# Kernel tuning notes

Hardware: AMD Instinct MI355X
Metric: run time of the kernel (lower is better)

Reference implementation:

```python
import jax, jax.numpy as jnp
import numpy as np

B, T, D, H = 512, 1024, 64, 64     # batch, time, input_size, hidden_size
R = 4                              # number of reward heads
MH = 32                            # MLP hidden size


def setup_inputs() -> dict:
    key = jax.random.key(0)
    ks = jax.random.split(key, 16)
    s = lambda k, shape, scale=1.0: jax.random.normal(k, shape, dtype=jnp.float32) * scale
    inp = {
        "x": s(ks[0], (B, T, D)),
        # learned initial states (nn.Parameter randn(1,1,H) -> store as (H,))
        "h_init": s(ks[1], (H,)),
        "c_init": s(ks[2], (H,)),
        # LSTM params, PyTorch layout: W_ih (4H, D), W_hh (4H, H), gate order i,f,g,o
        "W_ih": s(ks[3], (4 * H, D), 1.0 / np.sqrt(H)),
        "W_hh": s(ks[4], (4 * H, H), 1.0 / np.sqrt(H)),
        "b_ih": s(ks[5], (4 * H,), 1.0 / np.sqrt(H)),
        "b_hh": s(ks[6], (4 * H,), 1.0 / np.sqrt(H)),
        # R stacked MLP heads: Linear(H,MH) -> ReLU -> Linear(MH,MH) -> ReLU -> Linear(MH,1)
        "W1": s(ks[7], (R, MH, H), 1.0 / np.sqrt(H)),
        "b1": s(ks[8], (R, MH), 1.0 / np.sqrt(H)),
        "W2": s(ks[9], (R, MH, MH), 1.0 / np.sqrt(MH)),
        "b2": s(ks[10], (R, MH), 1.0 / np.sqrt(MH)),
        "W3": s(ks[11], (R, 1, MH), 1.0 / np.sqrt(MH)),
        "b3": s(ks[12], (R, 1), 1.0 / np.sqrt(MH)),
    }
    return inp


def _lstm(x, h0, c0, W_ih, W_hh, b_ih, b_hh):
    # x: (B, T, D). Returns y: (B, T, H).
    Hh = h0.shape[-1]
    b = b_ih + b_hh                      # (4H,)
    # precompute input projections for all steps: (T, B, 4H)
    xg = jnp.einsum('btd,gd->tbg', x, W_ih) + b

    def step(carry, xg_t):
        h, c = carry                     # (B, H) each
        gates = xg_t + h @ W_hh.T        # (B, 4H)
        i, f, g, o = jnp.split(gates, 4, axis=-1)
        c = jax.nn.sigmoid(f) * c + jax.nn.sigmoid(i) * jnp.tanh(g)
        h = jax.nn.sigmoid(o) * jnp.tanh(c)
        return (h, c), h

    Bb = x.shape[0]
    h0b = jnp.broadcast_to(h0, (Bb, Hh))
    c0b = jnp.broadcast_to(c0, (Bb, Hh))
    _, ys = jax.lax.scan(step, (h0b, c0b), xg)   # ys: (T, B, H)
    return jnp.transpose(ys, (1, 0, 2))


def _heads(y, W1, b1, W2, b2, W3, b3):
    # y: (B, T, H) -> (R, B, T); all R heads computed in one batched einsum chain
    h1 = jax.nn.relu(jnp.einsum('bth,rmh->rbtm', y, W1) + b1[:, None, None, :])
    h2 = jax.nn.relu(jnp.einsum('rbtm,rnm->rbtn', h1, W2) + b2[:, None, None, :])
    out = jnp.einsum('rbtn,ron->rbto', h2, W3) + b3[:, None, None, :]
    return out[..., 0]                   # squeeze last dim -> (R, B, T)


def reference(x, h_init, c_init, W_ih, W_hh, b_ih, b_hh, W1, b1, W2, b2, W3, b3):
    y = _lstm(x, h_init, c_init, W_ih, W_hh, b_ih, b_hh)
    outs = _heads(y, W1, b1, W2, b2, W3, b3)   # (R, B, T); row r == rewards[r] head
    return (y, outs)
```

## Files before the change

### kernel.cpp

```cpp
#include <hip/hip_runtime.h>

#define BB 512
#define TT 1024
#define DD 64
#define HH 64
#define G4 256
#define RR 4
#define MHH 32
#define BT (BB * TT)
#define Y_SIZE (BB * TT * HH)

typedef _Float16 half8 __attribute__((ext_vector_type(8)));
typedef _Float16 half4 __attribute__((ext_vector_type(4)));
typedef float f32x4 __attribute__((ext_vector_type(4)));

#define MFMA16(a, b, c) __builtin_amdgcn_mfma_f32_16x16x32_f16((a), (b), (c), 0, 0, 0)

__device__ __forceinline__ void wg_barrier_lds() {
    asm volatile("s_waitcnt lgkmcnt(0)" ::: "memory");
    __builtin_amdgcn_s_barrier();
    asm volatile("" ::: "memory");
}

__device__ __forceinline__ float sigm(float x) {
    return __builtin_amdgcn_rcpf(1.0f + __expf(-x));
}
__device__ __forceinline__ float tanh_(float x) {
    return 1.0f - 2.0f * __builtin_amdgcn_rcpf(1.0f + __expf(2.0f * x));
}

__device__ __forceinline__ half8 cvt8(f32x4 a, f32x4 b) {
    half8 h;
    h[0] = (_Float16)a[0]; h[1] = (_Float16)a[1];
    h[2] = (_Float16)a[2]; h[3] = (_Float16)a[3];
    h[4] = (_Float16)b[0]; h[5] = (_Float16)b[1];
    h[6] = (_Float16)b[2]; h[7] = (_Float16)b[3];
    return h;
}

__global__ __launch_bounds__(256) void lstm_kernel(
    const float* __restrict__ x, const float* __restrict__ h_init,
    const float* __restrict__ c_init, const float* __restrict__ W_ih,
    const float* __restrict__ W_hh, const float* __restrict__ b_ih,
    const float* __restrict__ b_hh, float* __restrict__ y)
{
    __shared__ alignas(16) _Float16 xch[2][16][2][DD];
    __shared__ alignas(16) _Float16 hst[2][2][HH];

    const int tid  = threadIdx.x;
    const int wave = tid >> 6;
    const int lane = tid & 63;
    const int col  = lane & 15;
    const int quad = lane >> 4;
    const int sel  = (lane >> 3) & 1;
    const int r_act = lane >> 5;
    const int j    = (wave << 4) + col;
    const bool writer = ((lane >> 4) & 1) == 0;

    const int b0 = blockIdx.x * 2;

    half8 bf[4][4];
    f32x4 biasv[4];
#pragma unroll
    for (int G = 0; G < 4; ++G) {
        const int n = (G << 6) + j;
        const float bs = b_ih[n] + b_hh[n];
        biasv[G][0] = bs; biasv[G][1] = bs; biasv[G][2] = bs; biasv[G][3] = bs;
#pragma unroll
        for (int c = 0; c < 4; ++c) {
            const float* src = (c < 2) ? (W_ih + n * DD + c * 32 + quad * 8)
                                       : (W_hh + n * HH + (c - 2) * 32 + quad * 8);
            f32x4 w0 = *(const f32x4*)src;
            f32x4 w1 = *(const f32x4*)(src + 4);
            bf[G][c] = cvt8(w0, w1);
        }
    }

    float c_state = c_init[j];

    if (tid < 128) {
        const int rr = tid >> 6, jj = tid & 63;
        hst[0][rr][jj] = (_Float16)h_init[jj];
    }
    {
        const int ss = tid >> 4, rr = (tid >> 3) & 1, j0 = (tid & 7) << 3;
        const float* src = x + ((b0 + rr) * TT + ss) * DD + j0;
        f32x4 g0 = *(const f32x4*)src;
        f32x4 g1 = *(const f32x4*)(src + 4);
        *(half8*)&xch[0][ss][rr][j0] = cvt8(g0, g1);
    }
    wg_barrier_lds();

    const int ss_pf = tid >> 4, rr_pf = (tid >> 3) & 1, j0_pf = (tid & 7) << 3;

    for (int ci = 0; ci < 64; ++ci) {
        const int buf = ci & 1;
        const bool pf = (ci + 1) < 64;
        f32x4 g0, g1;
        if (pf) {
            const float* src = x + ((b0 + rr_pf) * TT + ((ci + 1) << 4) + ss_pf) * DD + j0_pf;
            g0 = *(const f32x4*)src;
            g1 = *(const f32x4*)(src + 4);
        }
#pragma unroll
        for (int s = 0; s < 16; ++s) {
            const int t = (ci << 4) + s;
            const int p = s & 1;
            const _Float16* xrow = &xch[buf][s][sel][0];
            half8 a0 = *(const half8*)(xrow + quad * 8);
            half8 a1 = *(const half8*)(xrow + 32 + quad * 8);
            const _Float16* hrow = &hst[p][sel][0];
            half8 a2 = *(const half8*)(hrow + quad * 8);
            half8 a3 = *(const half8*)(hrow + 32 + quad * 8);

            f32x4 acc0 = MFMA16(a0, bf[0][0], biasv[0]);
            f32x4 acc1 = MFMA16(a0, bf[1][0], biasv[1]);
            f32x4 acc2 = MFMA16(a0, bf[2][0], biasv[2]);
            f32x4 acc3 = MFMA16(a0, bf[3][0], biasv[3]);
            acc0 = MFMA16(a1, bf[0][1], acc0); acc1 = MFMA16(a1, bf[1][1], acc1);
            acc2 = MFMA16(a1, bf[2][1], acc2); acc3 = MFMA16(a1, bf[3][1], acc3);
            acc0 = MFMA16(a2, bf[0][2], acc0); acc1 = MFMA16(a2, bf[1][2], acc1);
            acc2 = MFMA16(a2, bf[2][2], acc2); acc3 = MFMA16(a2, bf[3][2], acc3);
            acc0 = MFMA16(a3, bf[0][3], acc0); acc1 = MFMA16(a3, bf[1][3], acc1);
            acc2 = MFMA16(a3, bf[2][3], acc2); acc3 = MFMA16(a3, bf[3][3], acc3);

            const float si = sigm(acc0[0]);
            const float sf = sigm(acc1[0]);
            const float tg = tanh_(acc2[0]);
            const float so = sigm(acc3[0]);
            c_state = sf * c_state + si * tg;
            const float hv = so * tanh_(c_state);
            if (writer) {
                hst[p ^ 1][r_act][j] = (_Float16)hv;
                y[((b0 + r_act) * TT + t) * HH + j] = hv;
            }
            if (s == 15 && pf) {
                *(half8*)&xch[buf ^ 1][ss_pf][rr_pf][j0_pf] = cvt8(g0, g1);
            }
            wg_barrier_lds();
        }
    }
}

__global__ __launch_bounds__(256) void heads_kernel(
    const float* __restrict__ y,
    const float* __restrict__ W1, const float* __restrict__ b1,
    const float* __restrict__ W2, const float* __restrict__ b2,
    const float* __restrict__ W3, const float* __restrict__ b3,
    float* __restrict__ outs)
{
    __shared__ alignas(16) _Float16 ybuf[64][72];
    __shared__ alignas(16) _Float16 h1buf[64][136];
    __shared__ alignas(16) _Float16 h2buf[64][136];

    const int tid  = threadIdx.x;
    const int wave = tid >> 6;
    const int lane = tid & 63;
    const int col  = lane & 15;
    const int quad = lane >> 4;
    const int arow = (wave << 4) + col;

    half8 w1f[8][2]; float bias1[8];
#pragma unroll
    for (int nt = 0; nt < 8; ++nt) {
        const int n = nt * 16 + col;
        bias1[nt] = b1[n];
#pragma unroll
        for (int c = 0; c < 2; ++c) {
            const float* src = W1 + n * 64 + c * 32 + quad * 8;
            w1f[nt][c] = cvt8(*(const f32x4*)src, *(const f32x4*)(src + 4));
        }
    }
    half8 w2f[8]; float bias2[8];
#pragma unroll
    for (int nt = 0; nt < 8; ++nt) {
        const int n = nt * 16 + col;
        bias2[nt] = b2[n];
        const float* src = W2 + n * 32 + quad * 8;
        w2f[nt] = cvt8(*(const f32x4*)src, *(const f32x4*)(src + 4));
    }
    const int hd3 = tid >> 6, row3 = tid & 63;
    float w3r[32];
#pragma unroll
    for (int i = 0; i < 32; i += 4) {
        f32x4 v = *(const f32x4*)(W3 + hd3 * 32 + i);
        w3r[i] = v[0]; w3r[i + 1] = v[1]; w3r[i + 2] = v[2]; w3r[i + 3] = v[3];
    }
    const float b3v = b3[hd3];

    for (int st = 0; st < 4; ++st) {
        const long base_row = (long)blockIdx.x * 256 + st * 64;
#pragma unroll
        for (int jj = 0; jj < 4; ++jj) {
            const int off = (jj * 256 + tid) * 4;
            const int row = off >> 6, cc = off & 63;
            f32x4 v = *(const f32x4*)(y + base_row * 64 + off);
            half4 hv = {(_Float16)v[0], (_Float16)v[1], (_Float16)v[2], (_Float16)v[3]};
            *(half4*)&ybuf[row][cc] = hv;
        }
        wg_barrier_lds();

        half8 a0 = *(const half8*)&ybuf[arow][quad * 8];
        half8 a1 = *(const half8*)&ybuf[arow][32 + quad * 8];
#pragma unroll
        for (int nt = 0; nt < 8; ++nt) {
            f32x4 acc = {bias1[nt], bias1[nt], bias1[nt], bias1[nt]};
            acc = MFMA16(a0, w1f[nt][0], acc);
            acc = MFMA16(a1, w1f[nt][1], acc);
#pragma unroll
            for (int r = 0; r < 4; ++r) {
                float v = acc[r] > 0.0f ? acc[r] : 0.0f;
                h1buf[(wave << 4) + (quad << 2) + r][nt * 16 + col] = (_Float16)v;
            }
        }
        wg_barrier_lds();

        half8 ah[4];
#pragma unroll
        for (int hd = 0; hd < 4; ++hd)
            ah[hd] = *(const half8*)&h1buf[arow][hd * 32 + quad * 8];
#pragma unroll
        for (int nt = 0; nt < 8; ++nt) {
            f32x4 acc = {bias2[nt], bias2[nt], bias2[nt], bias2[nt]};
            acc = MFMA16(ah[nt >> 1], w2f[nt], acc);
#pragma unroll
            for (int r = 0; r < 4; ++r) {
                float v = acc[r] > 0.0f ? acc[r] : 0.0f;
                h2buf[(wave << 4) + (quad << 2) + r][nt * 16 + col] = (_Float16)v;
            }
        }
        wg_barrier_lds();

        float acc = b3v;
#pragma unroll
        for (int c = 0; c < 4; ++c) {
            half8 v = *(const half8*)&h2buf[row3][hd3 * 32 + c * 8];
#pragma unroll
            for (int u = 0; u < 8; ++u)
                acc = fmaf((float)v[u], w3r[c * 8 + u], acc);
        }
        outs[(long)hd3 * BT + base_row + row3] = acc;
        wg_barrier_lds();
    }
}

extern "C" void kernel_launch(void* const* d_in, const int* in_sizes, int n_in,
                              void* d_out, int out_size, void* d_ws, size_t ws_size,
                              hipStream_t stream) {
    (void)in_sizes; (void)n_in; (void)out_size; (void)d_ws; (void)ws_size;
    const float* x      = (const float*)d_in[0];
    const float* h_init = (const float*)d_in[1];
    const float* c_init = (const float*)d_in[2];
    const float* W_ih   = (const float*)d_in[3];
    const float* W_hh   = (const float*)d_in[4];
    const float* b_ih   = (const float*)d_in[5];
    const float* b_hh   = (const float*)d_in[6];
    const float* W1     = (const float*)d_in[7];
    const float* b1     = (const float*)d_in[8];
    const float* W2     = (const float*)d_in[9];
    const float* b2     = (const float*)d_in[10];
    const float* W3     = (const float*)d_in[11];
    const float* b3     = (const float*)d_in[12];
    float* y    = (float*)d_out;
    float* outs = y + Y_SIZE;

    lstm_kernel<<<dim3(256), dim3(256), 0, stream>>>(x, h_init, c_init, W_ih, W_hh,
                                                     b_ih, b_hh, y);
    heads_kernel<<<dim3(2048), dim3(256), 0, stream>>>(y, W1, b1, W2, b2, W3, b3, outs);
}
```

Baseline: 563.9 us.

## Hoist LSTM input projection per chunk and restructure heads kernel per-wave

The LSTM kernel now computes the input-projection MFMAs for a 16-step chunk up front into an LDS fp32 buffer, so each recurrent step only runs the four W_hh MFMAs on the critical path plus LDS reads of the precomputed gates. The x-chunk LDS rows are padded, and the prefetch store moves to step 14. The heads kernel is restructured so each wave processes its own rows with per-wave double-buffered LDS and no workgroup barriers. It loads y directly into registers with a one-tile prefetch, and the final W3 layer runs as an MFMA with zero-padded weights instead of scalar FMAs. This adds LDS usage and extra LDS traffic for the gate buffer.

```diff
diff --git a/kernel.cpp b/kernel.cpp
--- a/kernel.cpp
+++ b/kernel.cpp
@@ -4,9 +4,6 @@
 #define TT 1024
 #define DD 64
 #define HH 64
-#define G4 256
-#define RR 4
-#define MHH 32
 #define BT (BB * TT)
 #define Y_SIZE (BB * TT * HH)
 
@@ -44,8 +41,9 @@
     const float* __restrict__ W_hh, const float* __restrict__ b_ih,
     const float* __restrict__ b_hh, float* __restrict__ y)
 {
-    __shared__ alignas(16) _Float16 xch[2][16][2][DD];
+    __shared__ alignas(16) _Float16 xch[2][16][2][72];
     __shared__ alignas(16) _Float16 hst[2][2][HH];
+    __shared__ float xg[16][2][265];
 
     const int tid  = threadIdx.x;
     const int wave = tid >> 6;
@@ -102,25 +100,42 @@
             g0 = *(const f32x4*)src;
             g1 = *(const f32x4*)(src + 4);
         }
+
+#pragma unroll
+        for (int rr = 0; rr < 2; ++rr) {
+            half8 ax0 = *(const half8*)&xch[buf][col][rr][quad * 8];
+            half8 ax1 = *(const half8*)&xch[buf][col][rr][32 + quad * 8];
+#pragma unroll
+            for (int G = 0; G < 4; ++G) {
+                f32x4 d = MFMA16(ax0, bf[G][0], biasv[G]);
+                d = MFMA16(ax1, bf[G][1], d);
+#pragma unroll
+                for (int r = 0; r < 4; ++r)
+                    xg[(quad << 2) + r][rr][(G << 6) + j] = d[r];
+            }
+        }
+
 #pragma unroll
         for (int s = 0; s < 16; ++s) {
             const int t = (ci << 4) + s;
             const int p = s & 1;
-            const _Float16* xrow = &xch[buf][s][sel][0];
-            half8 a0 = *(const half8*)(xrow + quad * 8);
-            half8 a1 = *(const half8*)(xrow + 32 + quad * 8);
+
+            const float xg0 = xg[s][r_act][0 * 64 + j];
+            const float xg1 = xg[s][r_act][1 * 64 + j];
+            const float xg2 = xg[s][r_act][2 * 64 + j];
+            const float xg3 = xg[s][r_act][3 * 64 + j];
             const _Float16* hrow = &hst[p][sel][0];
             half8 a2 = *(const half8*)(hrow + quad * 8);
             half8 a3 = *(const half8*)(hrow + 32 + quad * 8);
 
-            f32x4 acc0 = MFMA16(a0, bf[0][0], biasv[0]);
-            f32x4 acc1 = MFMA16(a0, bf[1][0], biasv[1]);
-            f32x4 acc2 = MFMA16(a0, bf[2][0], biasv[2]);
-            f32x4 acc3 = MFMA16(a0, bf[3][0], biasv[3]);
-            acc0 = MFMA16(a1, bf[0][1], acc0); acc1 = MFMA16(a1, bf[1][1], acc1);
-            acc2 = MFMA16(a1, bf[2][1], acc2); acc3 = MFMA16(a1, bf[3][1], acc3);
-            acc0 = MFMA16(a2, bf[0][2], acc0); acc1 = MFMA16(a2, bf[1][2], acc1);
-            acc2 = MFMA16(a2, bf[2][2], acc2); acc3 = MFMA16(a2, bf[3][2], acc3);
+            f32x4 c0 = {xg0, xg0, xg0, xg0};
+            f32x4 c1 = {xg1, xg1, xg1, xg1};
+            f32x4 c2 = {xg2, xg2, xg2, xg2};
+            f32x4 c3 = {xg3, xg3, xg3, xg3};
+            f32x4 acc0 = MFMA16(a2, bf[0][2], c0);
+            f32x4 acc1 = MFMA16(a2, bf[1][2], c1);
+            f32x4 acc2 = MFMA16(a2, bf[2][2], c2);
+            f32x4 acc3 = MFMA16(a2, bf[3][2], c3);
             acc0 = MFMA16(a3, bf[0][3], acc0); acc1 = MFMA16(a3, bf[1][3], acc1);
             acc2 = MFMA16(a3, bf[2][3], acc2); acc3 = MFMA16(a3, bf[3][3], acc3);
 
@@ -134,7 +149,7 @@
                 hst[p ^ 1][r_act][j] = (_Float16)hv;
                 y[((b0 + r_act) * TT + t) * HH + j] = hv;
             }
-            if (s == 15 && pf) {
+            if (s == 14 && pf) {
                 *(half8*)&xch[buf ^ 1][ss_pf][rr_pf][j0_pf] = cvt8(g0, g1);
             }
             wg_barrier_lds();
@@ -149,16 +164,14 @@
     const float* __restrict__ W3, const float* __restrict__ b3,
     float* __restrict__ outs)
 {
-    __shared__ alignas(16) _Float16 ybuf[64][72];
-    __shared__ alignas(16) _Float16 h1buf[64][136];
-    __shared__ alignas(16) _Float16 h2buf[64][136];
+    __shared__ alignas(16) _Float16 h1w[4][2][16][144];
+    __shared__ alignas(16) _Float16 h2w[4][2][16][144];
 
     const int tid  = threadIdx.x;
     const int wave = tid >> 6;
     const int lane = tid & 63;
     const int col  = lane & 15;
     const int quad = lane >> 4;
-    const int arow = (wave << 4) + col;
 
     half8 w1f[8][2]; float bias1[8];
 #pragma unroll
@@ -179,29 +192,39 @@
         const float* src = W2 + n * 32 + quad * 8;
         w2f[nt] = cvt8(*(const f32x4*)src, *(const f32x4*)(src + 4));
     }
-    const int hd3 = tid >> 6, row3 = tid & 63;
-    float w3r[32];
-#pragma unroll
-    for (int i = 0; i < 32; i += 4) {
-        f32x4 v = *(const f32x4*)(W3 + hd3 * 32 + i);
-        w3r[i] = v[0]; w3r[i + 1] = v[1]; w3r[i + 2] = v[2]; w3r[i + 3] = v[3];
-    }
-    const float b3v = b3[hd3];
-
-    for (int st = 0; st < 4; ++st) {
-        const long base_row = (long)blockIdx.x * 256 + st * 64;
-#pragma unroll
-        for (int jj = 0; jj < 4; ++jj) {
-            const int off = (jj * 256 + tid) * 4;
-            const int row = off >> 6, cc = off & 63;
-            f32x4 v = *(const f32x4*)(y + base_row * 64 + off);
-            half4 hv = {(_Float16)v[0], (_Float16)v[1], (_Float16)v[2], (_Float16)v[3]};
-            *(half4*)&ybuf[row][cc] = hv;
-        }
-        wg_barrier_lds();
-
-        half8 a0 = *(const half8*)&ybuf[arow][quad * 8];
-        half8 a1 = *(const half8*)&ybuf[arow][32 + quad * 8];
+    half8 b3f[4];
+    {
+        const float* src = W3 + (col < 4 ? col * 32 : 0) + quad * 8;
+        half8 wv = cvt8(*(const f32x4*)src, *(const f32x4*)(src + 4));
+        half8 hz;
+#pragma unroll
+        for (int i = 0; i < 8; ++i) hz[i] = (_Float16)0.0f;
+#pragma unroll
+        for (int kc = 0; kc < 4; ++kc)
+            b3f[kc] = (col == kc) ? wv : hz;
+    }
+    const float b3v = (col < 4) ? b3[col] : 0.0f;
+
+    const long wbase = (long)blockIdx.x * 256 + wave * 64;
+
+    f32x4 ga0, ga1, ga2, ga3;
+    {
+        const float* src = y + (wbase + col) * 64 + quad * 8;
+        ga0 = *(const f32x4*)src;       ga1 = *(const f32x4*)(src + 4);
+        ga2 = *(const f32x4*)(src + 32); ga3 = *(const f32x4*)(src + 36);
+    }
+
+#pragma unroll
+    for (int tb = 0; tb < 4; ++tb) {
+        const int pb = tb & 1;
+        half8 a0 = cvt8(ga0, ga1);
+        half8 a1 = cvt8(ga2, ga3);
+        if (tb < 3) {
+            const float* src = y + (wbase + (tb + 1) * 16 + col) * 64 + quad * 8;
+            ga0 = *(const f32x4*)src;       ga1 = *(const f32x4*)(src + 4);
+            ga2 = *(const f32x4*)(src + 32); ga3 = *(const f32x4*)(src + 36);
+        }
+
 #pragma unroll
         for (int nt = 0; nt < 8; ++nt) {
             f32x4 acc = {bias1[nt], bias1[nt], bias1[nt], bias1[nt]};
@@ -210,15 +233,13 @@
 #pragma unroll
             for (int r = 0; r < 4; ++r) {
                 float v = acc[r] > 0.0f ? acc[r] : 0.0f;
-                h1buf[(wave << 4) + (quad << 2) + r][nt * 16 + col] = (_Float16)v;
-            }
-        }
-        wg_barrier_lds();
-
+                h1w[wave][pb][(quad << 2) + r][nt * 16 + col] = (_Float16)v;
+            }
+        }
         half8 ah[4];
 #pragma unroll
         for (int hd = 0; hd < 4; ++hd)
-            ah[hd] = *(const half8*)&h1buf[arow][hd * 32 + quad * 8];
+            ah[hd] = *(const half8*)&h1w[wave][pb][col][hd * 32 + quad * 8];
 #pragma unroll
         for (int nt = 0; nt < 8; ++nt) {
             f32x4 acc = {bias2[nt], bias2[nt], bias2[nt], bias2[nt]};
@@ -226,21 +247,17 @@
 #pragma unroll
             for (int r = 0; r < 4; ++r) {
                 float v = acc[r] > 0.0f ? acc[r] : 0.0f;
-                h2buf[(wave << 4) + (quad << 2) + r][nt * 16 + col] = (_Float16)v;
-            }
-        }
-        wg_barrier_lds();
-
-        float acc = b3v;
-#pragma unroll
-        for (int c = 0; c < 4; ++c) {
-            half8 v = *(const half8*)&h2buf[row3][hd3 * 32 + c * 8];
-#pragma unroll
-            for (int u = 0; u < 8; ++u)
-                acc = fmaf((float)v[u], w3r[c * 8 + u], acc);
-        }
-        outs[(long)hd3 * BT + base_row + row3] = acc;
-        wg_barrier_lds();
+                h2w[wave][pb][(quad << 2) + r][nt * 16 + col] = (_Float16)v;
+            }
+        }
+        f32x4 d = {b3v, b3v, b3v, b3v};
+#pragma unroll
+        for (int kc = 0; kc < 4; ++kc) {
+            half8 av = *(const half8*)&h2w[wave][pb][col][kc * 32 + quad * 8];
+            d = MFMA16(av, b3f[kc], d);
+        }
+        if (col < 4)
+            *(f32x4*)(outs + (long)col * BT + wbase + tb * 16 + quad * 4) = d;
     }
 }
 
```

Measured after the change: 567.3 us. About the same (+0.6%).
